# Kernel tuning notes

Measured on AMD Instinct MI355X. Metric: run time of the kernel, lower is better.

The kernel has to match this reference:

```python
import jax, jax.numpy as jnp
import numpy as np

N_NODES = 100000
N_EDGES = 1600000
IN_DIM, HID_DIM, OUT_DIM = 128, 128, 47
BN_EPS = 1e-5


def setup_inputs() -> dict:
    key = jax.random.key(0)
    ks = jax.random.split(key, 12)
    x = jax.random.normal(ks[0], (N_NODES, IN_DIM), dtype=jnp.float32)
    edge_index = jax.random.randint(ks[1], (2, N_EDGES), 0, N_NODES, dtype=jnp.int32)
    def glorot(k, fan_in, fan_out):
        s = jnp.sqrt(6.0 / (fan_in + fan_out))
        return jax.random.uniform(k, (fan_in, fan_out), jnp.float32, -s, s)
    return {
        "x": x,
        "edge_index": edge_index,
        "W0": glorot(ks[2], IN_DIM, HID_DIM), "b0": jnp.zeros((HID_DIM,), jnp.float32),
        "W1": glorot(ks[3], HID_DIM, HID_DIM), "b1": jnp.zeros((HID_DIM,), jnp.float32),
        "W2": glorot(ks[4], HID_DIM, OUT_DIM), "b2": jnp.zeros((OUT_DIM,), jnp.float32),
        "g0": jnp.ones((HID_DIM,), jnp.float32), "be0": jnp.zeros((HID_DIM,), jnp.float32),
        "g1": jnp.ones((HID_DIM,), jnp.float32), "be1": jnp.zeros((HID_DIM,), jnp.float32),
    }


def _gcn_norm(edge_index, n_nodes):
    # add self-loops, compute sym-normalized edge weights (PyG GCNConv default)
    loop = jnp.arange(n_nodes, dtype=edge_index.dtype)
    src = jnp.concatenate([edge_index[0], loop])
    dst = jnp.concatenate([edge_index[1], loop])
    deg = jax.ops.segment_sum(jnp.ones_like(dst, dtype=jnp.float32), dst,
                              num_segments=n_nodes)
    dinv = jnp.where(deg > 0, jax.lax.rsqrt(deg), 0.0)
    norm = dinv[src] * dinv[dst]  # [E + N]
    return src, dst, norm


def _conv(x, W, b, src, dst, norm, n_nodes):
    h = x @ W                                   # [N, d_out]
    msg = h[src] * norm[:, None]                # gather + scale
    out = jax.ops.segment_sum(msg, dst, num_segments=n_nodes)
    return out + b


def _batchnorm(h, gamma, beta):
    mean = jnp.mean(h, axis=0)
    var = jnp.mean(jnp.square(h - mean), axis=0)  # biased var (torch BN)
    return (h - mean) * jax.lax.rsqrt(var + BN_EPS) * gamma + beta


def reference(x, edge_index, W0, b0, W1, b1, W2, b2, g0, be0, g1, be1):
    n = x.shape[0]
    src, dst, norm = _gcn_norm(edge_index, n)
    h = _conv(x, W0, b0, src, dst, norm, n)
    h = jax.nn.relu(_batchnorm(h, g0, be0))     # dropout = identity (eval)
    h = _conv(h, W1, b1, src, dst, norm, n)
    h = jax.nn.relu(_batchnorm(h, g1, be1))
    h = _conv(h, W2, b2, src, dst, norm, n)
    return jax.nn.log_softmax(h, axis=-1)
```

## Files before the change

kernel.cpp:

```cpp
#include <hip/hip_runtime.h>
#include <math.h>

#define N_NODES 100000
#define N_EDGES 1600000
#define HID 128
#define OUTD 47
#define OSTR 48

#define NPB 128
#define NB 782
#define BCAP 2560
#define CHUNK 2048
#define NCHB 782
#define CWB 64

typedef short bf16x8 __attribute__((ext_vector_type(8)));
typedef float f32x4 __attribute__((ext_vector_type(4)));

__device__ inline unsigned short f2bf(float x) {
    union { float f; unsigned int u; } v; v.f = x;
    unsigned int r = v.u + 0x7fffu + ((v.u >> 16) & 1u);
    return (unsigned short)(r >> 16);
}
__device__ inline float bf_lo(unsigned int u) { return __uint_as_float(u << 16); }
__device__ inline float bf_hi(unsigned int u) { return __uint_as_float(u & 0xffff0000u); }

__device__ inline unsigned int cvt_pk_bf16(float lo, float hi) {
    unsigned int r;
    asm("v_cvt_pk_bf16_f32 %0, %1, %2" : "=v"(r) : "v"(lo), "v"(hi));
    return r;
}

__device__ inline unsigned int src_chunk(unsigned int s) {
    return (s * 42950u) >> 28;
}


__global__ __launch_bounds__(256) void binA_k(
    const int* __restrict__ src, const int* __restrict__ dst,
    int* __restrict__ gcur, unsigned int* __restrict__ binned,
    const float* __restrict__ W0, const float* __restrict__ W1, const float* __restrict__ W2,
    unsigned short* __restrict__ Wt0, unsigned short* __restrict__ Wt1,
    unsigned short* __restrict__ Wt2)
{
    __shared__ unsigned int sortedL[CHUNK];
    __shared__ unsigned short bucketOf[CHUNK];
    __shared__ int cntL[NB];
    __shared__ int excL[NB];
    __shared__ int curL[NB];
    __shared__ int gposL[NB];
    __shared__ int partial[256];

    int t = threadIdx.x;

    if (blockIdx.x >= NCHB) {
        int i = (blockIdx.x - NCHB) * 256 + t;
        if (i < 16384) {
            int n = i >> 7, k = i & 127;
            Wt0[i] = f2bf(W0[k * 128 + n]);
            Wt1[i] = f2bf(W1[k * 128 + n]);
        }
        if (i < 48 * 128) {
            int n = i >> 7, k = i & 127;
            Wt2[i] = (n < OUTD) ? f2bf(W2[k * OUTD + n]) : (unsigned short)0;
        }
        return;
    }

    int e0 = blockIdx.x * CHUNK;

    for (int i = t; i < NB; i += 256) cntL[i] = 0;
    __syncthreads();

    for (int i = t; i < CHUNK; i += 256) {
        int e = e0 + i;
        if (e < N_EDGES) atomicAdd(&cntL[dst[e] >> 7], 1);
    }
    __syncthreads();

    int b4 = t * 4;
    int c0 = (b4 + 0 < NB) ? cntL[b4 + 0] : 0;
    int c1 = (b4 + 1 < NB) ? cntL[b4 + 1] : 0;
    int c2 = (b4 + 2 < NB) ? cntL[b4 + 2] : 0;
    int c3 = (b4 + 3 < NB) ? cntL[b4 + 3] : 0;
    int lsum = c0 + c1 + c2 + c3;
    partial[t] = lsum;
    __syncthreads();
    for (int off = 1; off < 256; off <<= 1) {
        int x = (t >= off) ? partial[t - off] : 0;
        __syncthreads();
        partial[t] += x;
        __syncthreads();
    }
    int pbase = partial[t] - lsum;
    if (b4 + 0 < NB) { excL[b4 + 0] = pbase;                curL[b4 + 0] = pbase; }
    if (b4 + 1 < NB) { excL[b4 + 1] = pbase + c0;           curL[b4 + 1] = pbase + c0; }
    if (b4 + 2 < NB) { excL[b4 + 2] = pbase + c0 + c1;      curL[b4 + 2] = pbase + c0 + c1; }
    if (b4 + 3 < NB) { excL[b4 + 3] = pbase + c0 + c1 + c2; curL[b4 + 3] = pbase + c0 + c1 + c2; }
    __syncthreads();

    int tot = partial[255];

    for (int i = t; i < CHUNK; i += 256) {
        int e = e0 + i;
        if (e < N_EDGES) {
            int d = dst[e];
            int s = src[e];
            int bkt = d >> 7;
            int pos = atomicAdd(&curL[bkt], 1);
            sortedL[pos] = ((unsigned int)s << 7) | (unsigned int)(d & 127);
            bucketOf[pos] = (unsigned short)bkt;
        }
    }
    __syncthreads();

    for (int b = t; b < NB; b += 256) {
        int c = cntL[b];
        gposL[b] = c ? atomicAdd(&gcur[b], c) : 0;
    }
    __syncthreads();

    for (int i = t; i < tot; i += 256) {
        unsigned int r = sortedL[i];
        int bkt = bucketOf[i];
        binned[(size_t)bkt * BCAP + gposL[bkt] + (i - excL[bkt])] = r;
    }
}


__global__ __launch_bounds__(256) void binB_k(
    const unsigned int* __restrict__ binned, const int* __restrict__ gcur,
    int2* __restrict__ rowse, float* __restrict__ dinv, int* __restrict__ colv)
{
    __shared__ unsigned int recL[BCAP];
    __shared__ int colL[BCAP];
    __shared__ int hist[2048];
    __shared__ int partial[256];

    int b = blockIdx.x, t = threadIdx.x;
    int cnt = gcur[b];
    int base = b * BCAP;
    const unsigned int* rp = binned + (size_t)b * BCAP;

    for (int i = t; i < 2048; i += 256) hist[i] = 0;
    __syncthreads();

    for (int i = t; i < cnt; i += 256) {
        unsigned int r = rp[i];
        recL[i] = r;
        unsigned int key = ((r & 127u) << 4) | src_chunk(r >> 7);
        atomicAdd(&hist[key], 1);
    }
    __syncthreads();

    int base8 = t * 8;
    int v[8], lsum = 0;
#pragma unroll
    for (int j = 0; j < 8; j++) { v[j] = hist[base8 + j]; lsum += v[j]; }
    partial[t] = lsum;
    __syncthreads();
    for (int off = 1; off < 256; off <<= 1) {
        int x = (t >= off) ? partial[t - off] : 0;
        __syncthreads();
        partial[t] += x;
        __syncthreads();
    }
    int run = partial[t] - lsum;
#pragma unroll
    for (int j = 0; j < 8; j++) { hist[base8 + j] = run; run += v[j]; }
    __syncthreads();

    if (t < NPB) {
        int node = b * NPB + t;
        if (node < N_NODES) {
            int start = hist[t << 4];
            int end = (t < NPB - 1) ? hist[(t + 1) << 4] : cnt;
            rowse[node] = make_int2(base + start, base + end);
            dinv[node] = rsqrtf((float)(end - start + 1));
        }
    }
    __syncthreads();

    for (int i = t; i < cnt; i += 256) {
        unsigned int r = recL[i];
        unsigned int key = ((r & 127u) << 4) | src_chunk(r >> 7);
        int pos = atomicAdd(&hist[key], 1);
        colL[pos] = (int)(r >> 7);
    }
    __syncthreads();
    for (int i = t; i < cnt; i += 256) colv[base + i] = colL[i];
}


template <int ABF16, int MODE, int NT, int OBF16>
__global__ __launch_bounds__(256) void gemm_k(
    const void* __restrict__ Ap, const unsigned short* __restrict__ Wt,
    const float* __restrict__ bnSum, const float* __restrict__ bnSq,
    const float* __restrict__ gam, const float* __restrict__ bet,
    const float* __restrict__ dinv, void* __restrict__ Outp,
    int ncols, int ostride)
{
    __shared__ unsigned short WtL[NT * 16][136];
    __shared__ float2 sST[128];

    int t = threadIdx.x;
    if (MODE) {
        if (t < 128) {
            float s_ = 0.f, q_ = 0.f;
            for (int sl = 0; sl < 64; sl++) {
                s_ += bnSum[sl * 128 + t];
                q_ += bnSq[sl * 128 + t];
            }
            float mean = s_ * (1.0f / N_NODES);
            float var = q_ * (1.0f / N_NODES) - mean * mean;
            float inv = rsqrtf(var + 1e-5f);
            float s = gam[t] * inv;
            sST[t] = make_float2(s, bet[t] - mean * s);
        }
    }

    const int TOT = NT * 16 * 128;
    for (int e = t * 8; e < TOT; e += 256 * 8) {
        int n = e >> 7, k = e & 127;
        uint4 v = *(const uint4*)(Wt + e);
        *(uint4*)&WtL[n][k] = v;
    }
    __syncthreads();

    int wave = t >> 6, lane = t & 63;
    int quad = lane >> 4, m16 = lane & 15;
    int rbase = blockIdx.x * 128 + wave * 32;

    uint4 av[2][4];
#pragma unroll
    for (int rt = 0; rt < 2; rt++) {
        int row = rbase + rt * 16 + m16;
        bool rv = (row < N_NODES);
        if (ABF16) {
            const uint4* ap = (const uint4*)((const unsigned short*)Ap + (size_t)row * 128);
#pragma unroll
            for (int kc = 0; kc < 4; kc++)
                av[rt][kc] = rv ? ap[kc * 4 + quad] : make_uint4(0, 0, 0, 0);
        } else {
            const float4* ap = (const float4*)((const float*)Ap + (size_t)row * 128);
            float4 f[8];
#pragma unroll
            for (int kc = 0; kc < 4; kc++) {
                f[2 * kc]     = rv ? ap[kc * 8 + quad * 2]     : make_float4(0.f, 0.f, 0.f, 0.f);
                f[2 * kc + 1] = rv ? ap[kc * 8 + quad * 2 + 1] : make_float4(0.f, 0.f, 0.f, 0.f);
            }
#pragma unroll
            for (int kc = 0; kc < 4; kc++) {
                uint4 v;
                v.x = cvt_pk_bf16(f[2 * kc].x, f[2 * kc].y);
                v.y = cvt_pk_bf16(f[2 * kc].z, f[2 * kc].w);
                v.z = cvt_pk_bf16(f[2 * kc + 1].x, f[2 * kc + 1].y);
                v.w = cvt_pk_bf16(f[2 * kc + 1].z, f[2 * kc + 1].w);
                av[rt][kc] = v;
            }
        }
    }

    f32x4 acc[2][NT];
#pragma unroll
    for (int rt = 0; rt < 2; rt++)
#pragma unroll
        for (int ct = 0; ct < NT; ct++) acc[rt][ct] = (f32x4){0.f, 0.f, 0.f, 0.f};

#pragma unroll
    for (int kc = 0; kc < 4; kc++) {
        int kb = kc * 32 + quad * 8;
        bf16x8 afrag[2];
#pragma unroll
        for (int rt = 0; rt < 2; rt++) {
            if (MODE) {
                unsigned int uu[4] = {av[rt][kc].x, av[rt][kc].y, av[rt][kc].z, av[rt][kc].w};
                unsigned int* up = (unsigned int*)&afrag[rt];
#pragma unroll
                for (int i = 0; i < 4; i++) {
                    int k0 = kb + 2 * i;
                    float2 sa = sST[k0], sb = sST[k0 + 1];
                    float lo = fmaxf(bf_lo(uu[i]) * sa.x + sa.y, 0.f);
                    float hi = fmaxf(bf_hi(uu[i]) * sb.x + sb.y, 0.f);
                    up[i] = cvt_pk_bf16(lo, hi);
                }
            } else {
                afrag[rt] = *(bf16x8*)&av[rt][kc];
            }
        }
#pragma unroll
        for (int ct = 0; ct < NT; ct++) {
            bf16x8 bfrag = *(bf16x8*)&WtL[ct * 16 + m16][kb];
#pragma unroll
            for (int rt = 0; rt < 2; rt++)
                acc[rt][ct] = __builtin_amdgcn_mfma_f32_16x16x32_bf16(
                    afrag[rt], bfrag, acc[rt][ct], 0, 0, 0);
        }
    }

#pragma unroll
    for (int rt = 0; rt < 2; rt++)
#pragma unroll
        for (int r = 0; r < 4; r++) {
            int row = rbase + rt * 16 + quad * 4 + r;
            if (row < N_NODES) {
                float d = dinv[row];
#pragma unroll
                for (int ct = 0; ct < NT; ct++) {
                    int c = ct * 16 + m16;
                    if (c < ncols) {
                        float val = acc[rt][ct][r] * d;
                        if (OBF16)
                            ((unsigned short*)Outp)[(size_t)row * ostride + c] =
                                (unsigned short)cvt_pk_bf16(val, 0.f);
                        else
                            ((float*)Outp)[(size_t)row * ostride + c] = val;
                    }
                }
            }
        }
}


__global__ __launch_bounds__(256) void agg_k(
    const unsigned int* __restrict__ H, const int2* __restrict__ rowse,
    const int* __restrict__ colv, const float* __restrict__ dinv,
    const float* __restrict__ bias,
    float* __restrict__ bnPS, float* __restrict__ bnPQ,
    unsigned int* __restrict__ out)
{
    __shared__ float red[2][4][16][8];

    int t = threadIdx.x;
    int gw = (blockIdx.x * 256 + t) >> 6;
    int lane = t & 63;
    int w = t >> 6;
    int q = lane >> 4;
    int c = lane & 15;
    int2 se = rowse[gw];
    int rp = se.x, re = se.y;
    const uint4* H4 = (const uint4*)H;

    float a0 = 0.f, a1 = 0.f, a2 = 0.f, a3 = 0.f;
    float a4 = 0.f, a5 = 0.f, a6 = 0.f, a7 = 0.f;
    if (q == 0) {
        uint4 u = H4[(size_t)gw * 16 + c];
        a0 = bf_lo(u.x); a1 = bf_hi(u.x); a2 = bf_lo(u.y); a3 = bf_hi(u.y);
        a4 = bf_lo(u.z); a5 = bf_hi(u.z); a6 = bf_lo(u.w); a7 = bf_hi(u.w);
    }

    for (int j0 = rp; j0 < re; j0 += 64) {
        int idx = (j0 + lane < re) ? colv[j0 + lane] : 0;
        int n = min(64, re - j0);
        int nq = n >> 2;
        int t4 = 0;
        for (; t4 + 1 < nq; t4 += 2) {
            int sa = __shfl(idx, 4 * t4 + q);
            int sb = __shfl(idx, 4 * t4 + 4 + q);
            uint4 ua = H4[(size_t)sa * 16 + c];
            uint4 ub = H4[(size_t)sb * 16 + c];
            a0 += bf_lo(ua.x) + bf_lo(ub.x);
            a1 += bf_hi(ua.x) + bf_hi(ub.x);
            a2 += bf_lo(ua.y) + bf_lo(ub.y);
            a3 += bf_hi(ua.y) + bf_hi(ub.y);
            a4 += bf_lo(ua.z) + bf_lo(ub.z);
            a5 += bf_hi(ua.z) + bf_hi(ub.z);
            a6 += bf_lo(ua.w) + bf_lo(ub.w);
            a7 += bf_hi(ua.w) + bf_hi(ub.w);
        }
        if (t4 < nq) {
            int sa = __shfl(idx, 4 * t4 + q);
            uint4 ua = H4[(size_t)sa * 16 + c];
            a0 += bf_lo(ua.x); a1 += bf_hi(ua.x);
            a2 += bf_lo(ua.y); a3 += bf_hi(ua.y);
            a4 += bf_lo(ua.z); a5 += bf_hi(ua.z);
            a6 += bf_lo(ua.w); a7 += bf_hi(ua.w);
        }
        int rem = n & 3;
        if (rem) {
            int sa = __shfl(idx, (n - rem) + q);
            if (q < rem) {
                uint4 ua = H4[(size_t)sa * 16 + c];
                a0 += bf_lo(ua.x); a1 += bf_hi(ua.x);
                a2 += bf_lo(ua.y); a3 += bf_hi(ua.y);
                a4 += bf_lo(ua.z); a5 += bf_hi(ua.z);
                a6 += bf_lo(ua.w); a7 += bf_hi(ua.w);
            }
        }
    }

    a0 += __shfl_xor(a0, 16); a0 += __shfl_xor(a0, 32);
    a1 += __shfl_xor(a1, 16); a1 += __shfl_xor(a1, 32);
    a2 += __shfl_xor(a2, 16); a2 += __shfl_xor(a2, 32);
    a3 += __shfl_xor(a3, 16); a3 += __shfl_xor(a3, 32);
    a4 += __shfl_xor(a4, 16); a4 += __shfl_xor(a4, 32);
    a5 += __shfl_xor(a5, 16); a5 += __shfl_xor(a5, 32);
    a6 += __shfl_xor(a6, 16); a6 += __shfl_xor(a6, 32);
    a7 += __shfl_xor(a7, 16); a7 += __shfl_xor(a7, 32);

    if (q == 0) {
        float d = dinv[gw];
        float4 ba = ((const float4*)bias)[2 * c];
        float4 bb = ((const float4*)bias)[2 * c + 1];
        float vv[8];
        vv[0] = a0 * d + ba.x; vv[1] = a1 * d + ba.y;
        vv[2] = a2 * d + ba.z; vv[3] = a3 * d + ba.w;
        vv[4] = a4 * d + bb.x; vv[5] = a5 * d + bb.y;
        vv[6] = a6 * d + bb.z; vv[7] = a7 * d + bb.w;
        uint4 r;
        r.x = cvt_pk_bf16(vv[0], vv[1]);
        r.y = cvt_pk_bf16(vv[2], vv[3]);
        r.z = cvt_pk_bf16(vv[4], vv[5]);
        r.w = cvt_pk_bf16(vv[6], vv[7]);
        ((uint4*)out)[(size_t)gw * 16 + c] = r;
#pragma unroll
        for (int k = 0; k < 8; k++) {
            red[0][w][c][k] = vv[k];
            red[1][w][c][k] = vv[k] * vv[k];
        }
    }
    __syncthreads();

    {
        int part = t >> 7;
        int ch = t & 127;
        int cc = ch >> 3, k = ch & 7;
        float s = red[part][0][cc][k] + red[part][1][cc][k]
                + red[part][2][cc][k] + red[part][3][cc][k];
        atomicAdd((part ? bnPQ : bnPS) + (blockIdx.x & 63) * 128 + ch, s);
    }
}


__global__ __launch_bounds__(256) void agg_out_k(
    const unsigned int* __restrict__ H, const int2* __restrict__ rowse,
    const int* __restrict__ colv, const float* __restrict__ dinv,
    const float* __restrict__ b2, float* __restrict__ out)
{
    int gw = (blockIdx.x * 256 + threadIdx.x) >> 6;
    int lane = threadIdx.x & 63;
    if (gw >= N_NODES) return;
    int q = lane >> 4;
    int c = lane & 15;
    bool ld = c < 12;
    int2 se = rowse[gw];
    int rp = se.x, re = se.y;
    const uint2* H2 = (const uint2*)H;

    float a0 = 0.f, a1 = 0.f, a2 = 0.f, a3 = 0.f;
    if (q == 0 && ld) {
        uint2 u = H2[(size_t)gw * 12 + c];
        a0 = bf_lo(u.x); a1 = bf_hi(u.x); a2 = bf_lo(u.y); a3 = bf_hi(u.y);
    }

    for (int j0 = rp; j0 < re; j0 += 64) {
        int idx = (j0 + lane < re) ? colv[j0 + lane] : 0;
        int n = min(64, re - j0);
        int nq = n >> 2;
        int t4 = 0;
        for (; t4 + 1 < nq; t4 += 2) {
            int sa = __shfl(idx, 4 * t4 + q);
            int sb = __shfl(idx, 4 * t4 + 4 + q);
            if (ld) {
                uint2 ua = H2[(size_t)sa * 12 + c];
                uint2 ub = H2[(size_t)sb * 12 + c];
                a0 += bf_lo(ua.x) + bf_lo(ub.x);
                a1 += bf_hi(ua.x) + bf_hi(ub.x);
                a2 += bf_lo(ua.y) + bf_lo(ub.y);
                a3 += bf_hi(ua.y) + bf_hi(ub.y);
            }
        }
        if (t4 < nq) {
            int sa = __shfl(idx, 4 * t4 + q);
            if (ld) {
                uint2 ua = H2[(size_t)sa * 12 + c];
                a0 += bf_lo(ua.x); a1 += bf_hi(ua.x);
                a2 += bf_lo(ua.y); a3 += bf_hi(ua.y);
            }
        }
        int rem = n & 3;
        if (rem) {
            int sa = __shfl(idx, (n - rem) + q);
            if (q < rem && ld) {
                uint2 ua = H2[(size_t)sa * 12 + c];
                a0 += bf_lo(ua.x); a1 += bf_hi(ua.x);
                a2 += bf_lo(ua.y); a3 += bf_hi(ua.y);
            }
        }
    }

    a0 += __shfl_xor(a0, 16); a0 += __shfl_xor(a0, 32);
    a1 += __shfl_xor(a1, 16); a1 += __shfl_xor(a1, 32);
    a2 += __shfl_xor(a2, 16); a2 += __shfl_xor(a2, 32);
    a3 += __shfl_xor(a3, 16); a3 += __shfl_xor(a3, 32);

    float d = dinv[gw];
    int ch = c * 4;
    float v0 = -INFINITY, v1 = -INFINITY, v2 = -INFINITY, v3 = -INFINITY;
    if (ld) {
        v0 = a0 * d + b2[ch];
        v1 = a1 * d + b2[ch + 1];
        v2 = a2 * d + b2[ch + 2];
        if (ch + 3 < OUTD) v3 = a3 * d + b2[ch + 3];
    }
    float m = fmaxf(fmaxf(v0, v1), fmaxf(v2, v3));
    m = fmaxf(m, __shfl_xor(m, 1));
    m = fmaxf(m, __shfl_xor(m, 2));
    m = fmaxf(m, __shfl_xor(m, 4));
    m = fmaxf(m, __shfl_xor(m, 8));
    float e = 0.f;
    if (ld) {
        e = __expf(v0 - m) + __expf(v1 - m) + __expf(v2 - m);
        if (ch + 3 < OUTD) e += __expf(v3 - m);
    }
    float sum = e;
    sum += __shfl_xor(sum, 1);
    sum += __shfl_xor(sum, 2);
    sum += __shfl_xor(sum, 4);
    sum += __shfl_xor(sum, 8);
    float ls = logf(sum);
    if (q == 0 && ld) {
        float* op = out + (size_t)gw * OUTD + ch;
        op[0] = v0 - m - ls;
        op[1] = v1 - m - ls;
        op[2] = v2 - m - ls;
        if (ch + 3 < OUTD) op[3] = v3 - m - ls;
    }
}


extern "C" void kernel_launch(void* const* d_in, const int* in_sizes, int n_in,
                              void* d_out, int out_size, void* d_ws, size_t ws_size,
                              hipStream_t stream)
{
    const float* x   = (const float*)d_in[0];
    const int*   ei  = (const int*)d_in[1];
    const float* W0  = (const float*)d_in[2];
    const float* b0  = (const float*)d_in[3];
    const float* W1  = (const float*)d_in[4];
    const float* b1  = (const float*)d_in[5];
    const float* W2  = (const float*)d_in[6];
    const float* b2  = (const float*)d_in[7];
    const float* g0  = (const float*)d_in[8];
    const float* be0 = (const float*)d_in[9];
    const float* g1  = (const float*)d_in[10];
    const float* be1 = (const float*)d_in[11];
    const int* srcv = ei;
    const int* dstv = ei + N_EDGES;

    char* w = (char*)d_ws;
    unsigned int* H0 = (unsigned int*)w;  w += (size_t)N_NODES * 128 * 2;
    unsigned int* H1 = (unsigned int*)w;  w += (size_t)N_NODES * 128 * 2;
    unsigned int* Hf = (unsigned int*)w;  w += (size_t)N_NODES * OSTR * 2;
    unsigned int* binned = (unsigned int*)w; w += (size_t)NB * BCAP * 4;
    int* colv = (int*)w;        w += (size_t)NB * BCAP * 4;
    unsigned short* Wt0 = (unsigned short*)w; w += 16384 * 2;
    unsigned short* Wt1 = (unsigned short*)w; w += 16384 * 2;
    unsigned short* Wt2 = (unsigned short*)w; w += 48 * 128 * 2;
    int2* rowse = (int2*)w;     w += (size_t)N_NODES * 8;
    float* dinv = (float*)w;    w += (size_t)N_NODES * 4;
    int* gcur = (int*)w;        w += 784 * 4;
    float* bnP0S = (float*)w;   w += 64 * 128 * 4;
    float* bnP0Q = (float*)w;   w += 64 * 128 * 4;
    float* bnP1S = (float*)w;   w += 64 * 128 * 4;
    float* bnP1Q = (float*)w;   w += 64 * 128 * 4;

    int gb = (N_NODES + 127) / 128;
    int ab = (N_NODES * 64 + 255) / 256;

    hipMemsetAsync(gcur, 0, 784 * 4 + 4 * 64 * 128 * 4, stream);

    binA_k<<<NCHB + CWB, 256, 0, stream>>>(srcv, dstv, gcur, binned,
                                           W0, W1, W2, Wt0, Wt1, Wt2);
    binB_k<<<NB, 256, 0, stream>>>(binned, gcur, rowse, dinv, colv);

    gemm_k<0, 0, 8, 1><<<gb, 256, 0, stream>>>(x, Wt0, nullptr, nullptr, nullptr, nullptr,
                                               dinv, H0, 128, 128);
    agg_k<<<ab, 256, 0, stream>>>(H0, rowse, colv, dinv, b0, bnP0S, bnP0Q, H1);

    gemm_k<1, 1, 8, 1><<<gb, 256, 0, stream>>>(H1, Wt1, bnP0S, bnP0Q, g0, be0,
                                               dinv, H0, 128, 128);
    agg_k<<<ab, 256, 0, stream>>>(H0, rowse, colv, dinv, b1, bnP1S, bnP1Q, H1);

    gemm_k<1, 1, 3, 1><<<gb, 256, 0, stream>>>(H1, Wt2, bnP1S, bnP1Q, g1, be1,
                                               dinv, Hf, OUTD, OSTR);
    agg_out_k<<<ab, 256, 0, stream>>>(Hf, rowse, colv, dinv, b2, (float*)d_out);
}
```

Measured before the change: 411.1 us.

## Make aggregation kernel persistent and pad final-layer features to 64 columns

The hidden-layer aggregation kernel becomes grid-stride over groups of four nodes with a fixed grid of 2048 blocks. Batch-norm partial sums now accumulate in registers across groups, so each block does one shared-memory reduction and one round of atomics instead of one per four nodes. Separately, the final-layer feature buffer stride goes from 48 to 64 and the last GEMM computes 64 padded columns, giving aligned 128-byte rows for the gather. The padding adds extra GEMM work and memory traffic in exchange for that alignment.

```diff
diff --git a/kernel.cpp b/kernel.cpp
--- a/kernel.cpp
+++ b/kernel.cpp
@@ -5,7 +5,7 @@
 #define N_EDGES 1600000
 #define HID 128
 #define OUTD 47
-#define OSTR 48
+#define OSTR 64
 
 #define NPB 128
 #define NB 782
@@ -13,6 +13,8 @@
 #define CHUNK 2048
 #define NCHB 782
 #define CWB 64
+#define NAGB 2048
+#define NGRP 25000
 
 typedef short bf16x8 __attribute__((ext_vector_type(8)));
 typedef float f32x4 __attribute__((ext_vector_type(4)));
@@ -60,7 +62,7 @@
             Wt0[i] = f2bf(W0[k * 128 + n]);
             Wt1[i] = f2bf(W1[k * 128 + n]);
         }
-        if (i < 48 * 128) {
+        if (i < 64 * 128) {
             int n = i >> 7, k = i & 127;
             Wt2[i] = (n < OUTD) ? f2bf(W2[k * OUTD + n]) : (unsigned short)0;
         }
@@ -332,95 +334,107 @@
     __shared__ float red[2][4][16][8];
 
     int t = threadIdx.x;
-    int gw = (blockIdx.x * 256 + t) >> 6;
-    int lane = t & 63;
-    int w = t >> 6;
-    int q = lane >> 4;
-    int c = lane & 15;
-    int2 se = rowse[gw];
-    int rp = se.x, re = se.y;
+    int lane = t & 63, w = t >> 6;
+    int q = lane >> 4, c = lane & 15;
     const uint4* H4 = (const uint4*)H;
 
-    float a0 = 0.f, a1 = 0.f, a2 = 0.f, a3 = 0.f;
-    float a4 = 0.f, a5 = 0.f, a6 = 0.f, a7 = 0.f;
-    if (q == 0) {
-        uint4 u = H4[(size_t)gw * 16 + c];
-        a0 = bf_lo(u.x); a1 = bf_hi(u.x); a2 = bf_lo(u.y); a3 = bf_hi(u.y);
-        a4 = bf_lo(u.z); a5 = bf_hi(u.z); a6 = bf_lo(u.w); a7 = bf_hi(u.w);
-    }
-
-    for (int j0 = rp; j0 < re; j0 += 64) {
-        int idx = (j0 + lane < re) ? colv[j0 + lane] : 0;
-        int n = min(64, re - j0);
-        int nq = n >> 2;
-        int t4 = 0;
-        for (; t4 + 1 < nq; t4 += 2) {
-            int sa = __shfl(idx, 4 * t4 + q);
-            int sb = __shfl(idx, 4 * t4 + 4 + q);
-            uint4 ua = H4[(size_t)sa * 16 + c];
-            uint4 ub = H4[(size_t)sb * 16 + c];
-            a0 += bf_lo(ua.x) + bf_lo(ub.x);
-            a1 += bf_hi(ua.x) + bf_hi(ub.x);
-            a2 += bf_lo(ua.y) + bf_lo(ub.y);
-            a3 += bf_hi(ua.y) + bf_hi(ub.y);
-            a4 += bf_lo(ua.z) + bf_lo(ub.z);
-            a5 += bf_hi(ua.z) + bf_hi(ub.z);
-            a6 += bf_lo(ua.w) + bf_lo(ub.w);
-            a7 += bf_hi(ua.w) + bf_hi(ub.w);
-        }
-        if (t4 < nq) {
-            int sa = __shfl(idx, 4 * t4 + q);
-            uint4 ua = H4[(size_t)sa * 16 + c];
-            a0 += bf_lo(ua.x); a1 += bf_hi(ua.x);
-            a2 += bf_lo(ua.y); a3 += bf_hi(ua.y);
-            a4 += bf_lo(ua.z); a5 += bf_hi(ua.z);
-            a6 += bf_lo(ua.w); a7 += bf_hi(ua.w);
-        }
-        int rem = n & 3;
-        if (rem) {
-            int sa = __shfl(idx, (n - rem) + q);
-            if (q < rem) {
+    float4 ba = ((const float4*)bias)[2 * c];
+    float4 bb = ((const float4*)bias)[2 * c + 1];
+
+    float sreg[8] = {0.f, 0.f, 0.f, 0.f, 0.f, 0.f, 0.f, 0.f};
+    float qreg[8] = {0.f, 0.f, 0.f, 0.f, 0.f, 0.f, 0.f, 0.f};
+
+    for (int grp = blockIdx.x; grp < NGRP; grp += gridDim.x) {
+        int gw = grp * 4 + w;
+        int2 se = rowse[gw];
+        int rp = se.x, re = se.y;
+
+        float a0 = 0.f, a1 = 0.f, a2 = 0.f, a3 = 0.f;
+        float a4 = 0.f, a5 = 0.f, a6 = 0.f, a7 = 0.f;
+        if (q == 0) {
+            uint4 u = H4[(size_t)gw * 16 + c];
+            a0 = bf_lo(u.x); a1 = bf_hi(u.x); a2 = bf_lo(u.y); a3 = bf_hi(u.y);
+            a4 = bf_lo(u.z); a5 = bf_hi(u.z); a6 = bf_lo(u.w); a7 = bf_hi(u.w);
+        }
+
+        for (int j0 = rp; j0 < re; j0 += 64) {
+            int idx = (j0 + lane < re) ? colv[j0 + lane] : 0;
+            int n = min(64, re - j0);
+            int nq = n >> 2;
+            int t4 = 0;
+            for (; t4 + 1 < nq; t4 += 2) {
+                int sa = __shfl(idx, 4 * t4 + q);
+                int sb = __shfl(idx, 4 * t4 + 4 + q);
+                uint4 ua = H4[(size_t)sa * 16 + c];
+                uint4 ub = H4[(size_t)sb * 16 + c];
+                a0 += bf_lo(ua.x) + bf_lo(ub.x);
+                a1 += bf_hi(ua.x) + bf_hi(ub.x);
+                a2 += bf_lo(ua.y) + bf_lo(ub.y);
+                a3 += bf_hi(ua.y) + bf_hi(ub.y);
+                a4 += bf_lo(ua.z) + bf_lo(ub.z);
+                a5 += bf_hi(ua.z) + bf_hi(ub.z);
+                a6 += bf_lo(ua.w) + bf_lo(ub.w);
+                a7 += bf_hi(ua.w) + bf_hi(ub.w);
+            }
+            if (t4 < nq) {
+                int sa = __shfl(idx, 4 * t4 + q);
                 uint4 ua = H4[(size_t)sa * 16 + c];
                 a0 += bf_lo(ua.x); a1 += bf_hi(ua.x);
                 a2 += bf_lo(ua.y); a3 += bf_hi(ua.y);
                 a4 += bf_lo(ua.z); a5 += bf_hi(ua.z);
                 a6 += bf_lo(ua.w); a7 += bf_hi(ua.w);
             }
-        }
-    }
-
-    a0 += __shfl_xor(a0, 16); a0 += __shfl_xor(a0, 32);
-    a1 += __shfl_xor(a1, 16); a1 += __shfl_xor(a1, 32);
-    a2 += __shfl_xor(a2, 16); a2 += __shfl_xor(a2, 32);
-    a3 += __shfl_xor(a3, 16); a3 += __shfl_xor(a3, 32);
-    a4 += __shfl_xor(a4, 16); a4 += __shfl_xor(a4, 32);
-    a5 += __shfl_xor(a5, 16); a5 += __shfl_xor(a5, 32);
-    a6 += __shfl_xor(a6, 16); a6 += __shfl_xor(a6, 32);
-    a7 += __shfl_xor(a7, 16); a7 += __shfl_xor(a7, 32);
+            int rem = n & 3;
+            if (rem) {
+                int sa = __shfl(idx, (n - rem) + q);
+                if (q < rem) {
+                    uint4 ua = H4[(size_t)sa * 16 + c];
+                    a0 += bf_lo(ua.x); a1 += bf_hi(ua.x);
+                    a2 += bf_lo(ua.y); a3 += bf_hi(ua.y);
+                    a4 += bf_lo(ua.z); a5 += bf_hi(ua.z);
+                    a6 += bf_lo(ua.w); a7 += bf_hi(ua.w);
+                }
+            }
+        }
+
+        a0 += __shfl_xor(a0, 16); a0 += __shfl_xor(a0, 32);
+        a1 += __shfl_xor(a1, 16); a1 += __shfl_xor(a1, 32);
+        a2 += __shfl_xor(a2, 16); a2 += __shfl_xor(a2, 32);
+        a3 += __shfl_xor(a3, 16); a3 += __shfl_xor(a3, 32);
+        a4 += __shfl_xor(a4, 16); a4 += __shfl_xor(a4, 32);
+        a5 += __shfl_xor(a5, 16); a5 += __shfl_xor(a5, 32);
+        a6 += __shfl_xor(a6, 16); a6 += __shfl_xor(a6, 32);
+        a7 += __shfl_xor(a7, 16); a7 += __shfl_xor(a7, 32);
+
+        if (q == 0) {
+            float d = dinv[gw];
+            float vv[8];
+            vv[0] = a0 * d + ba.x; vv[1] = a1 * d + ba.y;
+            vv[2] = a2 * d + ba.z; vv[3] = a3 * d + ba.w;
+            vv[4] = a4 * d + bb.x; vv[5] = a5 * d + bb.y;
+            vv[6] = a6 * d + bb.z; vv[7] = a7 * d + bb.w;
+            uint4 r;
+            r.x = cvt_pk_bf16(vv[0], vv[1]);
+            r.y = cvt_pk_bf16(vv[2], vv[3]);
+            r.z = cvt_pk_bf16(vv[4], vv[5]);
+            r.w = cvt_pk_bf16(vv[6], vv[7]);
+            ((uint4*)out)[(size_t)gw * 16 + c] = r;
+#pragma unroll
+            for (int k = 0; k < 8; k++) {
+                sreg[k] += vv[k];
+                qreg[k] += vv[k] * vv[k];
+            }
+        }
+    }
 
     if (q == 0) {
-        float d = dinv[gw];
-        float4 ba = ((const float4*)bias)[2 * c];
-        float4 bb = ((const float4*)bias)[2 * c + 1];
-        float vv[8];
-        vv[0] = a0 * d + ba.x; vv[1] = a1 * d + ba.y;
-        vv[2] = a2 * d + ba.z; vv[3] = a3 * d + ba.w;
-        vv[4] = a4 * d + bb.x; vv[5] = a5 * d + bb.y;
-        vv[6] = a6 * d + bb.z; vv[7] = a7 * d + bb.w;
-        uint4 r;
-        r.x = cvt_pk_bf16(vv[0], vv[1]);
-        r.y = cvt_pk_bf16(vv[2], vv[3]);
-        r.z = cvt_pk_bf16(vv[4], vv[5]);
-        r.w = cvt_pk_bf16(vv[6], vv[7]);
-        ((uint4*)out)[(size_t)gw * 16 + c] = r;
 #pragma unroll
         for (int k = 0; k < 8; k++) {
-            red[0][w][c][k] = vv[k];
-            red[1][w][c][k] = vv[k] * vv[k];
-        }
-    }
-    __syncthreads();
-
+            red[0][w][c][k] = sreg[k];
+            red[1][w][c][k] = qreg[k];
+        }
+    }
+    __syncthreads();
     {
         int part = t >> 7;
         int ch = t & 127;
@@ -449,7 +463,7 @@
 
     float a0 = 0.f, a1 = 0.f, a2 = 0.f, a3 = 0.f;
     if (q == 0 && ld) {
-        uint2 u = H2[(size_t)gw * 12 + c];
+        uint2 u = H2[(size_t)gw * 16 + c];
         a0 = bf_lo(u.x); a1 = bf_hi(u.x); a2 = bf_lo(u.y); a3 = bf_hi(u.y);
     }
 
@@ -462,8 +476,8 @@
             int sa = __shfl(idx, 4 * t4 + q);
             int sb = __shfl(idx, 4 * t4 + 4 + q);
             if (ld) {
-                uint2 ua = H2[(size_t)sa * 12 + c];
-                uint2 ub = H2[(size_t)sb * 12 + c];
+                uint2 ua = H2[(size_t)sa * 16 + c];
+                uint2 ub = H2[(size_t)sb * 16 + c];
                 a0 += bf_lo(ua.x) + bf_lo(ub.x);
                 a1 += bf_hi(ua.x) + bf_hi(ub.x);
                 a2 += bf_lo(ua.y) + bf_lo(ub.y);
@@ -473,7 +487,7 @@
         if (t4 < nq) {
             int sa = __shfl(idx, 4 * t4 + q);
             if (ld) {
-                uint2 ua = H2[(size_t)sa * 12 + c];
+                uint2 ua = H2[(size_t)sa * 16 + c];
                 a0 += bf_lo(ua.x); a1 += bf_hi(ua.x);
                 a2 += bf_lo(ua.y); a3 += bf_hi(ua.y);
             }
@@ -482,7 +496,7 @@
         if (rem) {
             int sa = __shfl(idx, (n - rem) + q);
             if (q < rem && ld) {
-                uint2 ua = H2[(size_t)sa * 12 + c];
+                uint2 ua = H2[(size_t)sa * 16 + c];
                 a0 += bf_lo(ua.x); a1 += bf_hi(ua.x);
                 a2 += bf_lo(ua.y); a3 += bf_hi(ua.y);
             }
@@ -556,7 +570,7 @@
     int* colv = (int*)w;        w += (size_t)NB * BCAP * 4;
     unsigned short* Wt0 = (unsigned short*)w; w += 16384 * 2;
     unsigned short* Wt1 = (unsigned short*)w; w += 16384 * 2;
-    unsigned short* Wt2 = (unsigned short*)w; w += 48 * 128 * 2;
+    unsigned short* Wt2 = (unsigned short*)w; w += 64 * 128 * 2;
     int2* rowse = (int2*)w;     w += (size_t)N_NODES * 8;
     float* dinv = (float*)w;    w += (size_t)N_NODES * 4;
     int* gcur = (int*)w;        w += 784 * 4;
@@ -576,13 +590,13 @@
 
     gemm_k<0, 0, 8, 1><<<gb, 256, 0, stream>>>(x, Wt0, nullptr, nullptr, nullptr, nullptr,
                                                dinv, H0, 128, 128);
-    agg_k<<<ab, 256, 0, stream>>>(H0, rowse, colv, dinv, b0, bnP0S, bnP0Q, H1);
+    agg_k<<<NAGB, 256, 0, stream>>>(H0, rowse, colv, dinv, b0, bnP0S, bnP0Q, H1);
 
     gemm_k<1, 1, 8, 1><<<gb, 256, 0, stream>>>(H1, Wt1, bnP0S, bnP0Q, g0, be0,
                                                dinv, H0, 128, 128);
-    agg_k<<<ab, 256, 0, stream>>>(H0, rowse, colv, dinv, b1, bnP1S, bnP1Q, H1);
-
-    gemm_k<1, 1, 3, 1><<<gb, 256, 0, stream>>>(H1, Wt2, bnP1S, bnP1Q, g1, be1,
-                                               dinv, Hf, OUTD, OSTR);
+    agg_k<<<NAGB, 256, 0, stream>>>(H0, rowse, colv, dinv, b1, bnP1S, bnP1Q, H1);
+
+    gemm_k<1, 1, 4, 1><<<gb, 256, 0, stream>>>(H1, Wt2, bnP1S, bnP1Q, g1, be1,
+                                               dinv, Hf, 64, OSTR);
     agg_out_k<<<ab, 256, 0, stream>>>(Hf, rowse, colv, dinv, b2, (float*)d_out);
 }
```

New measurement: 440.8 us. 1.07x slower.
